# Optimization experiments

Measured on AMD Instinct MI355X. Metric: run time of the kernel, lower is better.

Reference implementation:

```python
import jax, jax.numpy as jnp
import numpy as np

NUM_LEVELS = 16
LEVEL_DIM = 2
BASE_RES = 32
PER_LEVEL_SCALE = 2.0
TABLE_SIZE = 2 ** 19  # padded size of every level's table
RES = np.array([int(BASE_RES * PER_LEVEL_SCALE ** i) for i in range(NUM_LEVELS)], dtype=np.float32)
SIZES = np.minimum(RES.astype(np.float64) ** 3, TABLE_SIZE).astype(np.float32)  # true table sizes
NEAR, FAR, NUM_SAMPLES = 0.1, 1.5, 64
N_RAYS = 16384


def _xavier(key, fin, fout):
    lim = float(np.sqrt(6.0 / (fin + fout)))
    return jax.random.uniform(key, (fin, fout), jnp.float32, -lim, lim)


def setup_inputs() -> dict:
    key = jax.random.key(0)
    ks = jax.random.split(key, 12)
    rays_o = jax.random.uniform(ks[0], (N_RAYS, 3), jnp.float32, -0.5, 0.5)
    d = jax.random.normal(ks[1], (N_RAYS, 3), jnp.float32)
    rays_d = d / jnp.linalg.norm(d, axis=-1, keepdims=True)
    tables = jax.random.uniform(ks[2], (NUM_LEVELS, TABLE_SIZE, LEVEL_DIM), jnp.float32, -1e-4, 1e-4)
    return {
        'rays_o': rays_o, 'rays_d': rays_d, 'tables': tables,
        'Wg0': _xavier(ks[3], 32, 64), 'bg0': jnp.zeros((64,), jnp.float32),
        'Wg1': _xavier(ks[4], 64, 64), 'bg1': jnp.zeros((64,), jnp.float32),
        'Wd': _xavier(ks[5], 64, 16), 'bd': jnp.zeros((16,), jnp.float32),
        'Wc0': _xavier(ks[6], 24, 64), 'bc0': jnp.zeros((64,), jnp.float32),
        'Wc1': _xavier(ks[7], 64, 64), 'bc1': jnp.zeros((64,), jnp.float32),
        'Wc2': _xavier(ks[8], 64, 64), 'bc2': jnp.zeros((64,), jnp.float32),
        'Wch': _xavier(ks[9], 64, 3), 'bch': jnp.zeros((3,), jnp.float32),
    }


def _hash_encode(pts, tables):
    # pts: [N, S, 3] in roughly [-1, 1]; tables: [L, T, 2]
    res = jnp.asarray(RES)            # [L]
    sizes = jnp.asarray(SIZES)        # [L]
    scaled = (pts[..., None, :] + 1.0) / 2.0 * (res[:, None] - 1.0)     # [N,S,L,3]
    scaled = jnp.clip(scaled, 0.0, res[:, None] - 1.0)
    # torch computes the flat index in float then .long() (truncation), then clamps to table size
    idx_f = scaled[..., 0] * res * res + scaled[..., 1] * res + scaled[..., 2]  # [N,S,L]
    idx = jnp.minimum(idx_f, sizes - 1.0).astype(jnp.int32)
    feats = tables[jnp.arange(NUM_LEVELS)[None, None, :], idx]          # [N,S,L,2]
    return feats.reshape(feats.shape[:-2] + (NUM_LEVELS * LEVEL_DIM,))  # [N,S,32]


def _sh_encode(d):
    # degree-4 encoder in the source only ever builds 9 features
    x, y, z = d[..., 0], d[..., 1], d[..., 2]
    return jnp.stack([jnp.full_like(x, 0.5), x, y, z,
                      x * y, x * z, y * z, x * x - y * y, 3.0 * z * z - 1.0], axis=-1)  # [N,9]


def reference(rays_o, rays_d, tables, Wg0, bg0, Wg1, bg1, Wd, bd,
              Wc0, bc0, Wc1, bc1, Wc2, bc2, Wch, bch):
    n = rays_o.shape[0]
    # --- stratified-free (eval mode) sampling along rays ---
    t = jnp.linspace(0.0, 1.0, NUM_SAMPLES, dtype=jnp.float32)
    z_vals = jnp.broadcast_to(NEAR + (FAR - NEAR) * t, (n, NUM_SAMPLES))           # [N,S]
    pts = rays_o[:, None, :] + rays_d[:, None, :] * z_vals[..., None]              # [N,S,3]
    # --- LoDAwareNeRF forward ---
    feats = _hash_encode(pts, tables)                                              # [N,S,32]
    h = jax.nn.relu(feats @ Wg0 + bg0)
    h = jax.nn.relu(h @ Wg1 + bg1)
    geo = h @ Wd + bd                                                              # [N,S,16]
    density = jax.nn.softplus(geo[..., 0] - 1.0)                                   # [N,S]
    geo_feat = geo[..., 1:]                                                        # [N,S,15]
    dir_f = jnp.broadcast_to(_sh_encode(rays_d)[:, None, :], (n, NUM_SAMPLES, 9))  # [N,S,9]
    c = jnp.concatenate([geo_feat, dir_f], axis=-1)                                # [N,S,24]
    c = jax.nn.relu(c @ Wc0 + bc0)
    c = jax.nn.relu(c @ Wc1 + bc1)
    c = jax.nn.relu(c @ Wc2 + bc2)
    color = jax.nn.sigmoid(c @ Wch + bch)                                          # [N,S,3]
    # --- volume rendering compositing ---
    dists = z_vals[..., 1:] - z_vals[..., :-1]
    dists = jnp.concatenate([dists, jnp.full_like(dists[..., :1], 1e10)], axis=-1)
    dists = dists * jnp.linalg.norm(rays_d, axis=-1, keepdims=True)
    alpha = 1.0 - jnp.exp(-density * dists)                                        # [N,S]
    T = jnp.cumprod(1.0 - alpha + 1e-10, axis=-1)
    T = jnp.concatenate([jnp.ones_like(T[..., :1]), T[..., :-1]], axis=-1)
    weights = alpha * T                                                            # [N,S]
    rgb = jnp.sum(weights[..., None] * color, axis=-2)                             # [N,3]
    depth = jnp.sum(weights * z_vals, axis=-1)                                     # [N]
    acc = jnp.sum(weights, axis=-1)                                                # [N]
    return rgb, depth, acc, weights
```

## Files before the change

### kernel.cpp

```cpp
#include <hip/hip_runtime.h>
#include <hip/hip_bf16.h>
#include <math.h>

typedef float  f32x4 __attribute__((ext_vector_type(4)));
typedef short  s16x8 __attribute__((ext_vector_type(8)));
typedef unsigned int u32x2 __attribute__((ext_vector_type(2)));
typedef unsigned int u32x4 __attribute__((ext_vector_type(4)));

constexpr int kNRays = 16384;
constexpr int kOffDepth   = kNRays * 3;
constexpr int kOffAcc     = kOffDepth + kNRays;
constexpr int kOffWeights = kOffAcc + kNRays;

constexpr int kWg0 = 0;
constexpr int kWg1 = 2048;
constexpr int kWd  = 6144;
constexpr int kWc0 = 7168;
constexpr int kWc1 = 9216;
constexpr int kWc2 = 13312;
constexpr int kWch = 17408;
constexpr int kWsTotal = 18432;
constexpr int kPrepTotal = kWsTotal + 32;

__device__ __forceinline__ ushort f2bf(float x) {
    unsigned u = __float_as_uint(x);
    return (ushort)((u + 0x7FFFu + ((u >> 16) & 1u)) >> 16);
}
__device__ __forceinline__ unsigned pk2(float lo, float hi) {
    __hip_bfloat162 h = __float22bfloat162_rn(float2{lo, hi});
    return *reinterpret_cast<unsigned*>(&h);
}
__device__ __forceinline__ unsigned pk2r(float lo, float hi) {
    unsigned p = pk2(lo, hi), r;
    asm("v_pk_max_i16 %0, %1, 0" : "=v"(r) : "v"(p));
    return r;
}
__device__ __forceinline__ float sel4(float v0, float v1, float v2, float v3, int s) {
    float a = (s & 1) ? v1 : v0;
    float b = (s & 1) ? v3 : v2;
    return (s & 2) ? b : a;
}
template<int CTRL, int RMASK>
__device__ __forceinline__ float dpp_mul(float x) {
    int t = __builtin_amdgcn_update_dpp(0x3f800000, __float_as_int(x), CTRL, RMASK, 0xF, false);
    return x * __int_as_float(t);
}
template<int CTRL, int RMASK>
__device__ __forceinline__ float dpp_add(float x) {
    int t = __builtin_amdgcn_update_dpp(0, __float_as_int(x), CTRL, RMASK, 0xF, false);
    return x + __int_as_float(t);
}
__device__ __forceinline__ float dpp_sum64(float v) {
    v = dpp_add<0x111, 0xF>(v);
    v = dpp_add<0x112, 0xF>(v);
    v = dpp_add<0x114, 0xF>(v);
    v = dpp_add<0x118, 0xF>(v);
    v = dpp_add<0x142, 0xA>(v);
    v = dpp_add<0x143, 0xC>(v);
    return __int_as_float(__builtin_amdgcn_readlane(__float_as_int(v), 63));
}

__global__ __launch_bounds__(256) void prep_weights(
    const float* __restrict__ Wg0, const float* __restrict__ Wg1,
    const float* __restrict__ Wd,  const float* __restrict__ Wc0,
    const float* __restrict__ Wc1, const float* __restrict__ Wc2,
    const float* __restrict__ Wch, const float* __restrict__ bc0,
    const float* __restrict__ tables, ushort* __restrict__ ws)
{
    const int i = blockIdx.x * 256 + threadIdx.x;
    if (i >= kPrepTotal) return;
    if (i >= kWsTotal) {
        const int t = i - kWsTotal;
        if (t < 16) {
            const unsigned szm1 = (t == 0) ? 32767u : (t == 1) ? 262143u : 524287u;
            const float2 v = ((const float2*)tables)[((size_t)t << 19) + szm1];
            ((unsigned*)(ws + kWsTotal))[t] = pk2(v.x, v.y);
        }
        return;
    }
    if (i < kWg1) {
        const int r = i;
        const int e = r & 7, l = (r >> 3) & 63, mt = r >> 9;
        const int g = (l >> 4) & 3, c = l & 15;
        const int fr = 8 * (e >> 1) + 2 * g + (e & 1);
        ws[i] = f2bf(Wg0[fr * 64 + 16 * mt + c]);
        return;
    }
    const float* W; int FIN, FOUT, KT, base; bool dperm = false, c0bias = false;
    if (i < kWd)       { W = Wg1; FIN = 64; FOUT = 64; KT = 2; base = kWg1; }
    else if (i < kWc0) { W = Wd;  FIN = 64; FOUT = 16; KT = 2; base = kWd; dperm = true; }
    else if (i < kWc1) { W = Wc0; FIN = 24; FOUT = 64; KT = 1; base = kWc0; c0bias = true; }
    else if (i < kWc2) { W = Wc1; FIN = 64; FOUT = 64; KT = 2; base = kWc1; }
    else if (i < kWch) { W = Wc2; FIN = 64; FOUT = 64; KT = 2; base = kWc2; }
    else               { W = Wch; FIN = 64; FOUT = 3;  KT = 2; base = kWch; }
    const int r = i - base;
    const int e = r & 7, l = (r >> 3) & 63, t = r >> 9;
    const int kt = t % KT, mt = t / KT;
    const int k = kt * 32 + ((l >> 4) << 3) + e;
    int j = mt * 16 + (l & 15);
    if (dperm) j = (j == 15) ? 0 : j + 1;
    float w = 0.0f;
    if (k < FIN && j < FOUT) w = W[k * FOUT + j];
    if (c0bias && k == 24 && j < FOUT) w = bc0[j];
    ws[i] = f2bf(w);
}

template<int KT, bool HASBIAS>
__device__ __forceinline__ void layer64(ushort* __restrict__ Xw,
                                        const ushort* __restrict__ Aws,
                                        const float* __restrict__ bias,
                                        const int* rp, const int* wa,
                                        int g, int lane) {
    s16x8 B[KT][4];
#pragma unroll
    for (int kt = 0; kt < KT; ++kt)
#pragma unroll
        for (int nt = 0; nt < 4; ++nt)
            B[kt][nt] = *(const s16x8*)&Xw[rp[kt * 4 + nt]];
#pragma unroll
    for (int mt = 0; mt < 4; ++mt) {
        const s16x8 A0 = *(const s16x8*)&Aws[((mt * KT + 0) * 64 + lane) * 8];
        s16x8 A1;
        if constexpr (KT == 2) A1 = *(const s16x8*)&Aws[((mt * KT + 1) * 64 + lane) * 8];
        f32x4 b;
        if constexpr (HASBIAS) b = *(const f32x4*)(bias + mt * 16 + g * 4);
        else                   b = (f32x4){ 0.f, 0.f, 0.f, 0.f };
        f32x4 acc[4];
#pragma unroll
        for (int nt = 0; nt < 4; ++nt) {
            acc[nt] = __builtin_amdgcn_mfma_f32_16x16x32_bf16(A0, B[0][nt], b, 0, 0, 0);
            if constexpr (KT == 2)
                acc[nt] = __builtin_amdgcn_mfma_f32_16x16x32_bf16(A1, B[1][nt], acc[nt], 0, 0, 0);
        }
#pragma unroll
        for (int nt = 0; nt < 4; ++nt)
            *(u32x2*)&Xw[wa[mt * 4 + nt]] =
                (u32x2){ pk2r(acc[nt].x, acc[nt].y), pk2r(acc[nt].z, acc[nt].w) };
    }
}

__device__ __forceinline__ void layer16(const ushort* __restrict__ Xw,
                                        const ushort* __restrict__ Aws,
                                        const int* rp, int lane, f32x4 acc[4]) {
    const s16x8 A0 = *(const s16x8*)&Aws[(0 * 64 + lane) * 8];
    const s16x8 A1 = *(const s16x8*)&Aws[(1 * 64 + lane) * 8];
#pragma unroll
    for (int nt = 0; nt < 4; ++nt) {
        const s16x8 B0 = *(const s16x8*)&Xw[rp[0 * 4 + nt]];
        acc[nt] = __builtin_amdgcn_mfma_f32_16x16x32_bf16(A0, B0, acc[nt], 0, 0, 0);
        const s16x8 B1 = *(const s16x8*)&Xw[rp[1 * 4 + nt]];
        acc[nt] = __builtin_amdgcn_mfma_f32_16x16x32_bf16(A1, B1, acc[nt], 0, 0, 0);
    }
}

__global__ __launch_bounds__(256, 4) void nerf_mfma_kernel(
    const float* __restrict__ rays_o, const float* __restrict__ rays_d,
    const float* __restrict__ tables, const ushort* __restrict__ ws,
    const float* __restrict__ bg0, const float* __restrict__ bg1,
    const float* __restrict__ bd,  const float* __restrict__ bc1,
    const float* __restrict__ bc2, const float* __restrict__ bch,
    float* __restrict__ out)
{
    __shared__ __align__(16) ushort Xs[4 * 4096];
    const int tid  = threadIdx.x;
    const int wid  = tid >> 6;
    const int lane = tid & 63;
    const int c16  = lane & 15;
    const int g    = lane >> 4;
    const int ray  = blockIdx.x * 4 + wid;
    ushort* Xw = Xs + wid * 4096;

    const float ox = rays_o[ray * 3 + 0], oy = rays_o[ray * 3 + 1], oz = rays_o[ray * 3 + 2];
    const float dx = rays_d[ray * 3 + 0], dy = rays_d[ray * 3 + 1], dz = rays_d[ray * 3 + 2];

    const float step = 1.0f / 63.0f;
    const float z  = 0.1f + 1.4f * ((float)lane * step);
    const float zn = 0.1f + 1.4f * ((float)(lane + 1) * step);

    int rp[8], wa[16];
#pragma unroll
    for (int kt = 0; kt < 2; ++kt)
#pragma unroll
        for (int nt = 0; nt < 4; ++nt)
            rp[kt * 4 + nt] = (nt * 16 + c16) * 64 + 8 * ((kt * 4 + g) ^ (c16 & 7));
#pragma unroll
    for (int mt = 0; mt < 4; ++mt)
#pragma unroll
        for (int nt = 0; nt < 4; ++nt)
            wa[mt * 4 + nt] = (nt * 16 + c16) * 64
                            + 8 * ((2 * mt + (g >> 1)) ^ (c16 & 7)) + 4 * (g & 1);

    const unsigned* cstp = (const unsigned*)(ws + kWsTotal);
    const unsigned cj1 = cstp[4 + g], cj2 = cstp[8 + g], cj3 = cstp[12 + g];

    const float pxm = fminf(fmaf(dx, 0.1f, ox), fmaf(dx, 1.5f, ox));
    const bool allhi = (pxm >= -0.98f);

    const float2* __restrict__ tb = (const float2*)tables;
    const float tc = (float)c16 * step;
    s16x8 B0f[4];
#pragma unroll
    for (int nt = 0; nt < 4; ++nt) {
        const float ts = tc + (float)nt * (16.0f / 63.0f);
        const float zs = fmaf(1.4f, ts, 0.1f);
        const float px = fmaf(dx, zs, ox), py = fmaf(dy, zs, oy), pz = fmaf(dz, zs, oz);
        u32x4 val;
        {
            const float res = (float)(32 << g);
            const float rm1 = res - 1.0f;
            const float hf = 0.5f * rm1;
            const float sx = __builtin_amdgcn_fmed3f(fmaf(px, hf, hf), 0.f, rm1);
            const float sy = __builtin_amdgcn_fmed3f(fmaf(py, hf, hf), 0.f, rm1);
            const float sz = __builtin_amdgcn_fmed3f(fmaf(pz, hf, hf), 0.f, rm1);
            const float idxf = fmaf(sx, res * res, fmaf(sy, res, sz));
            const float szm1 = (g == 0) ? 32767.f : (g == 1) ? 262143.f : 524287.f;
            const unsigned idx = (unsigned)(int)fminf(idxf, szm1);
            const float2 f2 = tb[((unsigned)g << 19) + idx];
            val[0] = pk2(f2.x, f2.y);
        }
        if (allhi) {
            val[1] = cj1; val[2] = cj2; val[3] = cj3;
        } else {
#pragma unroll
            for (int j = 1; j < 4; ++j) {
                const int lv = 4 * j + g;
                const float res = (float)(32 << lv);
                const float rm1 = res - 1.0f;
                const float hf = 0.5f * rm1;
                const float sx = __builtin_amdgcn_fmed3f(fmaf(px, hf, hf), 0.f, rm1);
                const float sy = __builtin_amdgcn_fmed3f(fmaf(py, hf, hf), 0.f, rm1);
                const float sz = __builtin_amdgcn_fmed3f(fmaf(pz, hf, hf), 0.f, rm1);
                const float idxf = fmaf(sx, res * res, fmaf(sy, res, sz));
                const int idx = (int)fminf(idxf, 524287.f);
                unsigned u;
                if (__any(idx != 524287)) {
                    const float2 f2 = tb[((unsigned)lv << 19) + (unsigned)idx];
                    u = pk2(f2.x, f2.y);
                } else {
                    u = (j == 1) ? cj1 : (j == 2) ? cj2 : cj3;
                }
                val[j] = u;
            }
        }
        B0f[nt] = *(const s16x8*)&val;
    }

#pragma unroll
    for (int mt = 0; mt < 4; ++mt) {
        const s16x8 A0 = *(const s16x8*)&ws[kWg0 + (mt * 64 + lane) * 8];
        const f32x4 b = *(const f32x4*)(bg0 + mt * 16 + g * 4);
        f32x4 acc[4];
#pragma unroll
        for (int nt = 0; nt < 4; ++nt)
            acc[nt] = __builtin_amdgcn_mfma_f32_16x16x32_bf16(A0, B0f[nt], b, 0, 0, 0);
#pragma unroll
        for (int nt = 0; nt < 4; ++nt)
            *(u32x2*)&Xw[wa[mt * 4 + nt]] =
                (u32x2){ pk2r(acc[nt].x, acc[nt].y), pk2r(acc[nt].z, acc[nt].w) };
    }

    layer64<2, true>(Xw, ws + kWg1, bg1, rp, wa, g, lane);

    f32x4 accd[4];
    {
        const float db0 = bd[g * 4 + 1];
        const float db1 = bd[g * 4 + 2];
        const float db2 = bd[g * 4 + 3];
        const float db3 = bd[(g == 3) ? 0 : g * 4 + 4];
        const f32x4 b = { db0, db1, db2, db3 };
#pragma unroll
        for (int nt = 0; nt < 4; ++nt) accd[nt] = b;
    }
    layer16(Xw, ws + kWd, rp, lane, accd);
    const float lgit = sel4(__shfl(accd[0].w, 48 + c16, 64),
                            __shfl(accd[1].w, 48 + c16, 64),
                            __shfl(accd[2].w, 48 + c16, 64),
                            __shfl(accd[3].w, 48 + c16, 64), g);
#pragma unroll
    for (int nt = 0; nt < 4; ++nt)
        *(u32x2*)&Xw[wa[nt]] = (u32x2){ pk2(accd[nt].x, accd[nt].y),
                                        pk2(accd[nt].z, accd[nt].w) };
    Xw[lane * 64 + 8 * (1 ^ (lane & 7)) + 7] = 0x3F00;
    {
        u32x4 w = { pk2(dx, dy), pk2(dz, dx * dy), pk2(dx * dz, dy * dz),
                    pk2(dx * dx - dy * dy, 3.f * dz * dz - 1.f) };
        *(u32x4*)&Xw[lane * 64 + 8 * (2 ^ (lane & 7))] = w;
    }
    {
        u32x4 w = { 0x00003F80u, 0u, 0u, 0u };
        *(u32x4*)&Xw[lane * 64 + 8 * (3 ^ (lane & 7))] = w;
    }

    layer64<1, false>(Xw, ws + kWc0, nullptr, rp, wa, g, lane);
    layer64<2, true >(Xw, ws + kWc1, bc1,     rp, wa, g, lane);
    layer64<2, true >(Xw, ws + kWc2, bc2,     rp, wa, g, lane);

    f32x4 accc[4];
    {
        const float cb0 = bch[0], cb1 = bch[1], cb2 = bch[2];
        const f32x4 b = (g == 0) ? (f32x4){ cb0, cb1, cb2, 0.f } : (f32x4){ 0.f, 0.f, 0.f, 0.f };
#pragma unroll
        for (int nt = 0; nt < 4; ++nt) accc[nt] = b;
    }
    layer16(Xw, ws + kWch, rp, lane, accc);
    const float lr  = sel4(__shfl(accc[0].x, c16, 64), __shfl(accc[1].x, c16, 64),
                           __shfl(accc[2].x, c16, 64), __shfl(accc[3].x, c16, 64), g);
    const float lgr = sel4(__shfl(accc[0].y, c16, 64), __shfl(accc[1].y, c16, 64),
                           __shfl(accc[2].y, c16, 64), __shfl(accc[3].y, c16, 64), g);
    const float lb  = sel4(__shfl(accc[0].z, c16, 64), __shfl(accc[1].z, c16, 64),
                           __shfl(accc[2].z, c16, 64), __shfl(accc[3].z, c16, 64), g);

    const float cr = 1.f / (1.f + __expf(-lr));
    const float cg = 1.f / (1.f + __expf(-lgr));
    const float cb = 1.f / (1.f + __expf(-lb));
    const float gx = lgit - 1.0f;
    const float density = fmaxf(gx, 0.f) + __logf(1.f + __expf(-fabsf(gx)));

    const float dnorm = sqrtf(dx * dx + dy * dy + dz * dz);
    float dist = (lane < 63) ? (zn - z) : 1e10f;
    dist *= dnorm;
    const float alpha = 1.0f - __expf(-density * dist);
    float f = 1.0f - alpha + 1e-10f;
    f = dpp_mul<0x111, 0xF>(f);
    f = dpp_mul<0x112, 0xF>(f);
    f = dpp_mul<0x114, 0xF>(f);
    f = dpp_mul<0x118, 0xF>(f);
    f = dpp_mul<0x142, 0xA>(f);
    f = dpp_mul<0x143, 0xC>(f);
    float T = __shfl_up(f, 1, 64);
    if (lane == 0) T = 1.0f;
    const float w = alpha * T;

    out[kOffWeights + ray * 64 + lane] = w;
    const float sr = dpp_sum64(w * cr);
    const float sg = dpp_sum64(w * cg);
    const float sb = dpp_sum64(w * cb);
    const float sd = dpp_sum64(w * z);
    const float sa = dpp_sum64(w);
    if (lane == 0) {
        out[ray * 3 + 0] = sr;
        out[ray * 3 + 1] = sg;
        out[ray * 3 + 2] = sb;
        out[kOffDepth + ray] = sd;
        out[kOffAcc + ray]   = sa;
    }
}

extern "C" void kernel_launch(void* const* d_in, const int* in_sizes, int n_in,
                              void* d_out, int out_size, void* d_ws, size_t ws_size,
                              hipStream_t stream) {
    const float* rays_o = (const float*)d_in[0];
    const float* rays_d = (const float*)d_in[1];
    const float* tables = (const float*)d_in[2];
    const float* Wg0 = (const float*)d_in[3];
    const float* bg0 = (const float*)d_in[4];
    const float* Wg1 = (const float*)d_in[5];
    const float* bg1 = (const float*)d_in[6];
    const float* Wd  = (const float*)d_in[7];
    const float* bd  = (const float*)d_in[8];
    const float* Wc0 = (const float*)d_in[9];
    const float* bc0 = (const float*)d_in[10];
    const float* Wc1 = (const float*)d_in[11];
    const float* bc1 = (const float*)d_in[12];
    const float* Wc2 = (const float*)d_in[13];
    const float* bc2 = (const float*)d_in[14];
    const float* Wch = (const float*)d_in[15];
    const float* bch = (const float*)d_in[16];
    float* out = (float*)d_out;
    ushort* wsp = (ushort*)d_ws;

    prep_weights<<<dim3((kPrepTotal + 255) / 256), dim3(256), 0, stream>>>(
        Wg0, Wg1, Wd, Wc0, Wc1, Wc2, Wch, bc0, tables, wsp);

    nerf_mfma_kernel<<<dim3(kNRays / 4), dim3(256), 0, stream>>>(
        rays_o, rays_d, tables, wsp,
        bg0, bg1, bd, bc1, bc2, bch, out);
}
```

Measured before the change: 66.34 us.

## Process two rays per wave and prefetch the second ray's hash gather

Each wave now handles two rays in sequence, and the grid is halved. The level-0..3 hash-table gather for the second ray is issued before the first ray's MLP runs, so its global-memory latency can overlap with MFMA work. Per-wave setup (LDS index tables, bias vectors, constants) is computed once and shared by both rays. The cost is higher register pressure from holding the prefetched values, and fewer blocks to hide latency with.

```diff
diff --git a/kernel.cpp b/kernel.cpp
--- a/kernel.cpp
+++ b/kernel.cpp
@@ -153,74 +153,48 @@
     }
 }
 
-__global__ __launch_bounds__(256, 4) void nerf_mfma_kernel(
-    const float* __restrict__ rays_o, const float* __restrict__ rays_d,
-    const float* __restrict__ tables, const ushort* __restrict__ ws,
-    const float* __restrict__ bg0, const float* __restrict__ bg1,
-    const float* __restrict__ bd,  const float* __restrict__ bc1,
-    const float* __restrict__ bc2, const float* __restrict__ bch,
-    float* __restrict__ out)
-{
-    __shared__ __align__(16) ushort Xs[4 * 4096];
-    const int tid  = threadIdx.x;
-    const int wid  = tid >> 6;
-    const int lane = tid & 63;
-    const int c16  = lane & 15;
-    const int g    = lane >> 4;
-    const int ray  = blockIdx.x * 4 + wid;
-    ushort* Xw = Xs + wid * 4096;
-
-    const float ox = rays_o[ray * 3 + 0], oy = rays_o[ray * 3 + 1], oz = rays_o[ray * 3 + 2];
-    const float dx = rays_d[ray * 3 + 0], dy = rays_d[ray * 3 + 1], dz = rays_d[ray * 3 + 2];
-
+__device__ __forceinline__ void gather_j0(const float2* __restrict__ tb,
+                                          float ox, float oy, float oz,
+                                          float dx, float dy, float dz,
+                                          int c16, int g, float2* __restrict__ f0) {
     const float step = 1.0f / 63.0f;
-    const float z  = 0.1f + 1.4f * ((float)lane * step);
-    const float zn = 0.1f + 1.4f * ((float)(lane + 1) * step);
-
-    int rp[8], wa[16];
-#pragma unroll
-    for (int kt = 0; kt < 2; ++kt)
-#pragma unroll
-        for (int nt = 0; nt < 4; ++nt)
-            rp[kt * 4 + nt] = (nt * 16 + c16) * 64 + 8 * ((kt * 4 + g) ^ (c16 & 7));
-#pragma unroll
-    for (int mt = 0; mt < 4; ++mt)
-#pragma unroll
-        for (int nt = 0; nt < 4; ++nt)
-            wa[mt * 4 + nt] = (nt * 16 + c16) * 64
-                            + 8 * ((2 * mt + (g >> 1)) ^ (c16 & 7)) + 4 * (g & 1);
-
-    const unsigned* cstp = (const unsigned*)(ws + kWsTotal);
-    const unsigned cj1 = cstp[4 + g], cj2 = cstp[8 + g], cj3 = cstp[12 + g];
-
-    const float pxm = fminf(fmaf(dx, 0.1f, ox), fmaf(dx, 1.5f, ox));
-    const bool allhi = (pxm >= -0.98f);
-
-    const float2* __restrict__ tb = (const float2*)tables;
     const float tc = (float)c16 * step;
-    s16x8 B0f[4];
 #pragma unroll
     for (int nt = 0; nt < 4; ++nt) {
         const float ts = tc + (float)nt * (16.0f / 63.0f);
         const float zs = fmaf(1.4f, ts, 0.1f);
         const float px = fmaf(dx, zs, ox), py = fmaf(dy, zs, oy), pz = fmaf(dz, zs, oz);
+        const float res = (float)(32 << g);
+        const float rm1 = res - 1.0f;
+        const float hf = 0.5f * rm1;
+        const float sx = __builtin_amdgcn_fmed3f(fmaf(px, hf, hf), 0.f, rm1);
+        const float sy = __builtin_amdgcn_fmed3f(fmaf(py, hf, hf), 0.f, rm1);
+        const float sz = __builtin_amdgcn_fmed3f(fmaf(pz, hf, hf), 0.f, rm1);
+        const float idxf = fmaf(sx, res * res, fmaf(sy, res, sz));
+        const float szm1 = (g == 0) ? 32767.f : (g == 1) ? 262143.f : 524287.f;
+        const unsigned idx = (unsigned)(int)fminf(idxf, szm1);
+        f0[nt] = tb[((unsigned)g << 19) + idx];
+    }
+}
+
+__device__ __forceinline__ void make_B0(const float2* __restrict__ tb,
+                                        float ox, float oy, float oz,
+                                        float dx, float dy, float dz,
+                                        bool allhi, const float2* __restrict__ f0,
+                                        unsigned cj1, unsigned cj2, unsigned cj3,
+                                        int c16, int g, s16x8* __restrict__ B0f) {
+    const float step = 1.0f / 63.0f;
+    const float tc = (float)c16 * step;
+#pragma unroll
+    for (int nt = 0; nt < 4; ++nt) {
         u32x4 val;
-        {
-            const float res = (float)(32 << g);
-            const float rm1 = res - 1.0f;
-            const float hf = 0.5f * rm1;
-            const float sx = __builtin_amdgcn_fmed3f(fmaf(px, hf, hf), 0.f, rm1);
-            const float sy = __builtin_amdgcn_fmed3f(fmaf(py, hf, hf), 0.f, rm1);
-            const float sz = __builtin_amdgcn_fmed3f(fmaf(pz, hf, hf), 0.f, rm1);
-            const float idxf = fmaf(sx, res * res, fmaf(sy, res, sz));
-            const float szm1 = (g == 0) ? 32767.f : (g == 1) ? 262143.f : 524287.f;
-            const unsigned idx = (unsigned)(int)fminf(idxf, szm1);
-            const float2 f2 = tb[((unsigned)g << 19) + idx];
-            val[0] = pk2(f2.x, f2.y);
-        }
+        val[0] = pk2(f0[nt].x, f0[nt].y);
         if (allhi) {
             val[1] = cj1; val[2] = cj2; val[3] = cj3;
         } else {
+            const float ts = tc + (float)nt * (16.0f / 63.0f);
+            const float zs = fmaf(1.4f, ts, 0.1f);
+            const float px = fmaf(dx, zs, ox), py = fmaf(dy, zs, oy), pz = fmaf(dz, zs, oz);
 #pragma unroll
             for (int j = 1; j < 4; ++j) {
                 const int lv = 4 * j + g;
@@ -244,7 +218,21 @@
         }
         B0f[nt] = *(const s16x8*)&val;
     }
-
+}
+
+__device__ __forceinline__ void run_ray(ushort* __restrict__ Xw,
+                                        const ushort* __restrict__ ws,
+                                        const float* __restrict__ bg0,
+                                        const float* __restrict__ bg1,
+                                        const float* __restrict__ bc1,
+                                        const float* __restrict__ bc2,
+                                        const f32x4 bdv, const f32x4 bchv,
+                                        const int* rp, const int* wa,
+                                        int g, int c16, int lane,
+                                        int ray, float dx, float dy, float dz,
+                                        float z, float zn,
+                                        const s16x8* __restrict__ B0f,
+                                        float* __restrict__ out) {
 #pragma unroll
     for (int mt = 0; mt < 4; ++mt) {
         const s16x8 A0 = *(const s16x8*)&ws[kWg0 + (mt * 64 + lane) * 8];
@@ -262,15 +250,8 @@
     layer64<2, true>(Xw, ws + kWg1, bg1, rp, wa, g, lane);
 
     f32x4 accd[4];
-    {
-        const float db0 = bd[g * 4 + 1];
-        const float db1 = bd[g * 4 + 2];
-        const float db2 = bd[g * 4 + 3];
-        const float db3 = bd[(g == 3) ? 0 : g * 4 + 4];
-        const f32x4 b = { db0, db1, db2, db3 };
-#pragma unroll
-        for (int nt = 0; nt < 4; ++nt) accd[nt] = b;
-    }
+#pragma unroll
+    for (int nt = 0; nt < 4; ++nt) accd[nt] = bdv;
     layer16(Xw, ws + kWd, rp, lane, accd);
     const float lgit = sel4(__shfl(accd[0].w, 48 + c16, 64),
                             __shfl(accd[1].w, 48 + c16, 64),
@@ -296,12 +277,8 @@
     layer64<2, true >(Xw, ws + kWc2, bc2,     rp, wa, g, lane);
 
     f32x4 accc[4];
-    {
-        const float cb0 = bch[0], cb1 = bch[1], cb2 = bch[2];
-        const f32x4 b = (g == 0) ? (f32x4){ cb0, cb1, cb2, 0.f } : (f32x4){ 0.f, 0.f, 0.f, 0.f };
-#pragma unroll
-        for (int nt = 0; nt < 4; ++nt) accc[nt] = b;
-    }
+#pragma unroll
+    for (int nt = 0; nt < 4; ++nt) accc[nt] = bchv;
     layer16(Xw, ws + kWch, rp, lane, accc);
     const float lr  = sel4(__shfl(accc[0].x, c16, 64), __shfl(accc[1].x, c16, 64),
                            __shfl(accc[2].x, c16, 64), __shfl(accc[3].x, c16, 64), g);
@@ -344,6 +321,75 @@
         out[kOffDepth + ray] = sd;
         out[kOffAcc + ray]   = sa;
     }
+}
+
+__global__ __launch_bounds__(256, 4) void nerf_mfma_kernel(
+    const float* __restrict__ rays_o, const float* __restrict__ rays_d,
+    const float* __restrict__ tables, const ushort* __restrict__ ws,
+    const float* __restrict__ bg0, const float* __restrict__ bg1,
+    const float* __restrict__ bd,  const float* __restrict__ bc1,
+    const float* __restrict__ bc2, const float* __restrict__ bch,
+    float* __restrict__ out)
+{
+    __shared__ __align__(16) ushort Xs[4 * 4096];
+    const int tid  = threadIdx.x;
+    const int wid  = tid >> 6;
+    const int lane = tid & 63;
+    const int c16  = lane & 15;
+    const int g    = lane >> 4;
+    ushort* Xw = Xs + wid * 4096;
+    const int ray0 = blockIdx.x * 8 + wid * 2;
+
+    const float step = 1.0f / 63.0f;
+    const float z  = 0.1f + 1.4f * ((float)lane * step);
+    const float zn = 0.1f + 1.4f * ((float)(lane + 1) * step);
+
+    int rp[8], wa[16];
+#pragma unroll
+    for (int kt = 0; kt < 2; ++kt)
+#pragma unroll
+        for (int nt = 0; nt < 4; ++nt)
+            rp[kt * 4 + nt] = (nt * 16 + c16) * 64 + 8 * ((kt * 4 + g) ^ (c16 & 7));
+#pragma unroll
+    for (int mt = 0; mt < 4; ++mt)
+#pragma unroll
+        for (int nt = 0; nt < 4; ++nt)
+            wa[mt * 4 + nt] = (nt * 16 + c16) * 64
+                            + 8 * ((2 * mt + (g >> 1)) ^ (c16 & 7)) + 4 * (g & 1);
+
+    const unsigned* cstp = (const unsigned*)(ws + kWsTotal);
+    const unsigned cj1 = cstp[4 + g], cj2 = cstp[8 + g], cj3 = cstp[12 + g];
+
+    const f32x4 bdv = { bd[g * 4 + 1], bd[g * 4 + 2], bd[g * 4 + 3],
+                        bd[(g == 3) ? 0 : g * 4 + 4] };
+    const f32x4 bchv = (g == 0) ? (f32x4){ bch[0], bch[1], bch[2], 0.f }
+                                : (f32x4){ 0.f, 0.f, 0.f, 0.f };
+
+    const float2* __restrict__ tb = (const float2*)tables;
+
+    const float oxA = rays_o[ray0 * 3 + 0], oyA = rays_o[ray0 * 3 + 1], ozA = rays_o[ray0 * 3 + 2];
+    const float dxA = rays_d[ray0 * 3 + 0], dyA = rays_d[ray0 * 3 + 1], dzA = rays_d[ray0 * 3 + 2];
+    float2 f0A[4];
+    gather_j0(tb, oxA, oyA, ozA, dxA, dyA, dzA, c16, g, f0A);
+    const bool hiA = fminf(fmaf(dxA, 0.1f, oxA), fmaf(dxA, 1.5f, oxA)) >= -0.98f;
+
+    const int rayB = ray0 + 1;
+    const float oxB = rays_o[rayB * 3 + 0], oyB = rays_o[rayB * 3 + 1], ozB = rays_o[rayB * 3 + 2];
+    const float dxB = rays_d[rayB * 3 + 0], dyB = rays_d[rayB * 3 + 1], dzB = rays_d[rayB * 3 + 2];
+
+    s16x8 B0f[4];
+    make_B0(tb, oxA, oyA, ozA, dxA, dyA, dzA, hiA, f0A, cj1, cj2, cj3, c16, g, B0f);
+
+    float2 f0B[4];
+    gather_j0(tb, oxB, oyB, ozB, dxB, dyB, dzB, c16, g, f0B);
+    const bool hiB = fminf(fmaf(dxB, 0.1f, oxB), fmaf(dxB, 1.5f, oxB)) >= -0.98f;
+
+    run_ray(Xw, ws, bg0, bg1, bc1, bc2, bdv, bchv, rp, wa, g, c16, lane,
+            ray0, dxA, dyA, dzA, z, zn, B0f, out);
+
+    make_B0(tb, oxB, oyB, ozB, dxB, dyB, dzB, hiB, f0B, cj1, cj2, cj3, c16, g, B0f);
+    run_ray(Xw, ws, bg0, bg1, bc1, bc2, bdv, bchv, rp, wa, g, c16, lane,
+            rayB, dxB, dyB, dzB, z, zn, B0f, out);
 }
 
 extern "C" void kernel_launch(void* const* d_in, const int* in_sizes, int n_in,
@@ -372,7 +418,7 @@
     prep_weights<<<dim3((kPrepTotal + 255) / 256), dim3(256), 0, stream>>>(
         Wg0, Wg1, Wd, Wc0, Wc1, Wc2, Wch, bc0, tables, wsp);
 
-    nerf_mfma_kernel<<<dim3(kNRays / 4), dim3(256), 0, stream>>>(
+    nerf_mfma_kernel<<<dim3(kNRays / 8), dim3(256), 0, stream>>>(
         rays_o, rays_d, tables, wsp,
         bg0, bg1, bd, bc1, bc2, bch, out);
 }
```

New measurement: 78.20 us. 1.18x slower.
